# Optimization experiments

Hardware: AMD Instinct MI355X
Metric: run time of the kernel (lower is better)

## Reference

```python
import jax, jax.numpy as jnp
import numpy as np
from jax import lax

BIG = 1e8  # sentinel 'infinity'; safe in fp32 since max (i-j)^2 ~ 512^2


def _dt1d(f, axis):
    """Exact 1-D squared-distance transform along `axis`:
    d[i] = min_j (i-j)^2 + f[j]. Scanned over j (min-plus), fully vectorized
    over all other dims."""
    f = jnp.moveaxis(f, axis, -1)
    shp = f.shape
    n = shp[-1]
    fr = f.reshape(-1, n)  # [R, n]
    idx = jnp.arange(n, dtype=f.dtype)

    def step(d, xs):
        fj, j = xs  # fj: [R], j: scalar position
        cand = fj[:, None] + (idx - j) ** 2  # [R, n]
        return jnp.minimum(d, cand), None

    d0 = jnp.full_like(fr, BIG)
    d, _ = lax.scan(step, d0, (fr.T, idx))
    return jnp.moveaxis(d.reshape(shp), -1, axis)


def _edt(mask):
    """Exact Euclidean distance transform: distance from every element to the
    nearest True element of `mask` (0 where mask is True). Matches
    scipy.ndimage.distance_transform_edt(~mask applied as in the torch module)
    via the exact separable squared-distance decomposition, over ALL dims
    (including batch/channel, as the original code does)."""
    f = jnp.where(mask, 0.0, BIG).astype(jnp.float32)
    for ax in range(f.ndim):
        f = _dt1d(f, ax)
    return jnp.sqrt(f)


def setup_inputs() -> dict:
    key = jax.random.key(0)
    k1, k2 = jax.random.split(key)
    shape = (8, 1, 512, 512)
    x = jax.random.normal(k1, shape, dtype=jnp.float32)
    # sparse binary label mask (~1/64 foreground) for non-trivial distances
    y = (jax.random.randint(k2, shape, 0, 64) == 0).astype(jnp.int32)
    return {"x": x, "y": y}


def reference(x, y):
    # original: dist = EDT(logical_not(y)) = distance to nearest nonzero of y
    d = _edt(y != 0)
    return (jax.nn.sigmoid(x) * d).mean()
```

## Files before the change

kernel.cpp:

```cpp
#include <hip/hip_runtime.h>
#include <math.h>

#define BIGV  1.0e8f
#define PLANE (512 * 512)
#define NTOT  (8 * PLANE)
#define PROWS 640
#define PSTRIDE (PROWS * 512)
#define HSENT 1023

__global__ __launch_bounds__(512) void dt_axis3(const int* __restrict__ y,
                                                unsigned short* __restrict__ g1u) {
    int blk = blockIdx.x;
    if (blk >= 4096) {
        int idx = (blk - 4096) * 512 + threadIdx.x;
        int plane = idx >> 16;
        int rem   = idx & 65535;
        int r     = rem >> 9;
        int c     = rem & 511;
        int row   = (r < 64) ? r : (r + 512);
        g1u[plane * PSTRIDE + row * 512 + c] = HSENT;
        return;
    }
    __shared__ unsigned long long words[8];
    int i = threadIdx.x;
    int e = blk * 512 + i;
    unsigned long long bal = __ballot(y[e] != 0);
    int wid  = i >> 6;
    int lane = i & 63;
    if (lane == 0) words[wid] = bal;
    __syncthreads();

    int k = wid, b = lane;
    int dr = 1 << 30;
    {
        unsigned long long m0 = words[k] & (~0ull << b);
        if (m0) {
            dr = (__ffsll((long long)m0) - 1) - b;
        } else {
            #pragma unroll
            for (int k2 = 0; k2 < 8; ++k2) {
                if (k2 > k && dr == (1 << 30) && words[k2]) {
                    dr = (k2 << 6) + (__ffsll((long long)words[k2]) - 1) - i;
                }
            }
        }
    }
    int dl = 1 << 30;
    {
        unsigned long long m0 = words[k] & (~0ull >> (63 - b));
        if (m0) {
            dl = b - (63 - __clzll((long long)m0));
        } else {
            #pragma unroll
            for (int k2 = 7; k2 >= 0; --k2) {
                if (k2 < k && dl == (1 << 30) && words[k2]) {
                    dl = i - ((k2 << 6) + 63 - __clzll((long long)words[k2]));
                }
            }
        }
    }
    int d = min(dl, dr);
    int h = min(d, HSENT);
    int bb = blk >> 9, i2 = blk & 511;
    g1u[bb * PSTRIDE + (64 + i2) * 512 + i] = (unsigned short)h;
}

__device__ inline double wave_reduce_d(double v) {
    #pragma unroll
    for (int off = 32; off > 0; off >>= 1) v += __shfl_down(v, off, 64);
    return v;
}

__global__ __launch_bounds__(256) void dt2_axis0_epilogue(
        const unsigned short* __restrict__ g1u,
        const float* __restrict__ x,
        double* __restrict__ partials) {
    int s  = blockIdx.x * 256 + threadIdx.x;
    int i2 = s >> 9;
    int i3 = s & 511;

    float v[8];
    #pragma unroll
    for (int bb = 0; bb < 8; ++bb) {
        const unsigned short* base = g1u + bb * PSTRIDE + (64 + i2) * 512 + i3;
        int h0  = base[0];
        float m = (float)(h0 * h0);
        int au = base[-512];
        int ad = base[+512];
        const unsigned short* up = base - 512;
        const unsigned short* dn = base + 512;
        float fr2 = 1.0f, dstep = 3.0f;
        int r = 1;
        for (; r < 64; ++r) {
            if (fr2 >= m) break;
            int hm = min(au, ad);
            float cand = (float)(hm * hm) + fr2;
            au = up[-512]; ad = dn[+512];
            up -= 512; dn += 512;
            m = fminf(m, cand);
            fr2 += dstep; dstep += 2.0f;
        }
        if (r == 64) {
            for (; r < 512; ++r) {
                float f2 = (float)(r * r);
                if (f2 >= m) break;
                int upr = i2 - r, dnr = i2 + r;
                if (upr < 0 && dnr >= 512) break;
                if (upr >= 0) {
                    int hh = g1u[bb * PSTRIDE + (64 + upr) * 512 + i3];
                    m = fminf(m, (float)(hh * hh) + f2);
                }
                if (dnr < 512) {
                    int hh = g1u[bb * PSTRIDE + (64 + dnr) * 512 + i3];
                    m = fminf(m, (float)(hh * hh) + f2);
                }
            }
        }
        v[bb] = m;
    }

    double acc = 0.0;
    #pragma unroll
    for (int b = 0; b < 8; ++b) {
        float m = BIGV;
        #pragma unroll
        for (int bp = 0; bp < 8; ++bp) {
            float db = (float)((b - bp) * (b - bp));
            m = fminf(m, v[bp] + db);
        }
        float xv  = x[b * PLANE + s];
        float sig = 1.0f / (1.0f + expf(-xv));
        acc += (double)(sig * sqrtf(m));
    }

    __shared__ double lds[4];
    double w = wave_reduce_d(acc);
    int lane = threadIdx.x & 63;
    int wid  = threadIdx.x >> 6;
    if (lane == 0) lds[wid] = w;
    __syncthreads();
    if (wid == 0) {
        double t = (lane < 4) ? lds[lane] : 0.0;
        #pragma unroll
        for (int off = 2; off > 0; off >>= 1) t += __shfl_down(t, off, 64);
        if (lane == 0) partials[blockIdx.x] = t;
    }
}

__global__ __launch_bounds__(256) void finalize(const double* __restrict__ partials,
                                                float* __restrict__ out) {
    double a = 0.0;
    for (int i = threadIdx.x; i < 1024; i += 256) a += partials[i];
    __shared__ double lds[4];
    double w = wave_reduce_d(a);
    int lane = threadIdx.x & 63;
    int wid  = threadIdx.x >> 6;
    if (lane == 0) lds[wid] = w;
    __syncthreads();
    if (threadIdx.x == 0) {
        double total = lds[0] + lds[1] + lds[2] + lds[3];
        out[0] = (float)(total / (double)NTOT);
    }
}

extern "C" void kernel_launch(void* const* d_in, const int* in_sizes, int n_in,
                              void* d_out, int out_size, void* d_ws, size_t ws_size,
                              hipStream_t stream) {
    const float* x = (const float*)d_in[0];
    const int*   y = (const int*)d_in[1];
    float* out = (float*)d_out;

    unsigned short* g1u = (unsigned short*)d_ws;
    double* partials = (double*)((char*)d_ws + (size_t)8 * PSTRIDE * sizeof(unsigned short));

    dt_axis3<<<5120, 512, 0, stream>>>(y, g1u);
    dt2_axis0_epilogue<<<PLANE / 256, 256, 0, stream>>>(g1u, x, partials);
    finalize<<<1, 256, 0, stream>>>(partials, out);
}
```

Baseline: 105.9 us.

## Parallelize column scan across batch planes with one thread per plane

The column distance-transform kernel now gives each of the 8 batch planes its own thread (32 pixels by 8 planes per block) instead of looping over the planes serially in one thread. The per-plane minima are exchanged through shared memory so the batch-axis transform and epilogue can run per plane. This gives 8x more threads to hide the latency of the dependent column scans, and a warp's 32 contiguous pixels still coalesce within each plane. In exchange it adds an extra barrier, more partial sums (8192) for the finalize kernel to read, and divergence inside each wave, which now spans two planes.

Measured after the change: 98.92 us. 1.07x faster.

```diff
diff --git a/kernel.cpp b/kernel.cpp
--- a/kernel.cpp
+++ b/kernel.cpp
@@ -75,63 +75,61 @@
         const unsigned short* __restrict__ g1u,
         const float* __restrict__ x,
         double* __restrict__ partials) {
-    int s  = blockIdx.x * 256 + threadIdx.x;
-    int i2 = s >> 9;
-    int i3 = s & 511;
+    int t   = threadIdx.x;
+    int pix = t & 31;
+    int bb  = t >> 5;
+    int s   = blockIdx.x * 32 + pix;
+    int i2  = s >> 9;
+    int i3  = s & 511;
 
-    float v[8];
-    #pragma unroll
-    for (int bb = 0; bb < 8; ++bb) {
-        const unsigned short* base = g1u + bb * PSTRIDE + (64 + i2) * 512 + i3;
-        int h0  = base[0];
-        float m = (float)(h0 * h0);
-        int au = base[-512];
-        int ad = base[+512];
-        const unsigned short* up = base - 512;
-        const unsigned short* dn = base + 512;
-        float fr2 = 1.0f, dstep = 3.0f;
-        int r = 1;
-        for (; r < 64; ++r) {
-            if (fr2 >= m) break;
-            int hm = min(au, ad);
-            float cand = (float)(hm * hm) + fr2;
-            au = up[-512]; ad = dn[+512];
-            up -= 512; dn += 512;
-            m = fminf(m, cand);
-            fr2 += dstep; dstep += 2.0f;
-        }
-        if (r == 64) {
-            for (; r < 512; ++r) {
-                float f2 = (float)(r * r);
-                if (f2 >= m) break;
-                int upr = i2 - r, dnr = i2 + r;
-                if (upr < 0 && dnr >= 512) break;
-                if (upr >= 0) {
-                    int hh = g1u[bb * PSTRIDE + (64 + upr) * 512 + i3];
-                    m = fminf(m, (float)(hh * hh) + f2);
-                }
-                if (dnr < 512) {
-                    int hh = g1u[bb * PSTRIDE + (64 + dnr) * 512 + i3];
-                    m = fminf(m, (float)(hh * hh) + f2);
-                }
+    const unsigned short* base = g1u + bb * PSTRIDE + (64 + i2) * 512 + i3;
+    int h0  = base[0];
+    float m = (float)(h0 * h0);
+    int au = base[-512];
+    int ad = base[+512];
+    const unsigned short* up = base - 512;
+    const unsigned short* dn = base + 512;
+    float fr2 = 1.0f, dstep = 3.0f;
+    int r = 1;
+    for (; r < 64; ++r) {
+        if (fr2 >= m) break;
+        int hm = min(au, ad);
+        float cand = (float)(hm * hm) + fr2;
+        au = up[-512]; ad = dn[+512];
+        up -= 512; dn += 512;
+        m = fminf(m, cand);
+        fr2 += dstep; dstep += 2.0f;
+    }
+    if (r == 64) {
+        for (; r < 512; ++r) {
+            float f2 = (float)(r * r);
+            if (f2 >= m) break;
+            int upr = i2 - r, dnr = i2 + r;
+            if (upr < 0 && dnr >= 512) break;
+            if (upr >= 0) {
+                int hh = g1u[bb * PSTRIDE + (64 + upr) * 512 + i3];
+                m = fminf(m, (float)(hh * hh) + f2);
+            }
+            if (dnr < 512) {
+                int hh = g1u[bb * PSTRIDE + (64 + dnr) * 512 + i3];
+                m = fminf(m, (float)(hh * hh) + f2);
             }
         }
-        v[bb] = m;
     }
 
-    double acc = 0.0;
+    __shared__ float vlds[32 * 9];
+    vlds[pix * 9 + bb] = m;
+    __syncthreads();
+
+    float mb = BIGV;
     #pragma unroll
-    for (int b = 0; b < 8; ++b) {
-        float m = BIGV;
-        #pragma unroll
-        for (int bp = 0; bp < 8; ++bp) {
-            float db = (float)((b - bp) * (b - bp));
-            m = fminf(m, v[bp] + db);
-        }
-        float xv  = x[b * PLANE + s];
-        float sig = 1.0f / (1.0f + expf(-xv));
-        acc += (double)(sig * sqrtf(m));
+    for (int bp = 0; bp < 8; ++bp) {
+        float db = (float)((bb - bp) * (bb - bp));
+        mb = fminf(mb, vlds[pix * 9 + bp] + db);
     }
+    float xv  = x[bb * PLANE + s];
+    float sig = 1.0f / (1.0f + expf(-xv));
+    double acc = (double)(sig * sqrtf(mb));
 
     __shared__ double lds[4];
     double w = wave_reduce_d(acc);
@@ -140,17 +138,17 @@
     if (lane == 0) lds[wid] = w;
     __syncthreads();
     if (wid == 0) {
-        double t = (lane < 4) ? lds[lane] : 0.0;
+        double tt = (lane < 4) ? lds[lane] : 0.0;
         #pragma unroll
-        for (int off = 2; off > 0; off >>= 1) t += __shfl_down(t, off, 64);
-        if (lane == 0) partials[blockIdx.x] = t;
+        for (int off = 2; off > 0; off >>= 1) tt += __shfl_down(tt, off, 64);
+        if (lane == 0) partials[blockIdx.x] = tt;
     }
 }
 
 __global__ __launch_bounds__(256) void finalize(const double* __restrict__ partials,
                                                 float* __restrict__ out) {
     double a = 0.0;
-    for (int i = threadIdx.x; i < 1024; i += 256) a += partials[i];
+    for (int i = threadIdx.x; i < 8192; i += 256) a += partials[i];
     __shared__ double lds[4];
     double w = wave_reduce_d(a);
     int lane = threadIdx.x & 63;
@@ -174,6 +172,6 @@
     double* partials = (double*)((char*)d_ws + (size_t)8 * PSTRIDE * sizeof(unsigned short));
 
     dt_axis3<<<5120, 512, 0, stream>>>(y, g1u);
-    dt2_axis0_epilogue<<<PLANE / 256, 256, 0, stream>>>(g1u, x, partials);
+    dt2_axis0_epilogue<<<PLANE / 32, 256, 0, stream>>>(g1u, x, partials);
     finalize<<<1, 256, 0, stream>>>(partials, out);
 }
```
